# Performance work log

Measured on AMD Instinct MI355X. Metric: run time of the kernel, lower is better.

## Reference

```python
import jax, jax.numpy as jnp
import numpy as np

BRANCH = 8
DEPTH = 4
BATCH = 8192


def _build_tree(b=BRANCH, depth=DEPTH):
    level_sizes = [b ** l for l in range(depth + 1)]
    offsets = np.cumsum([0] + level_sizes)
    E = int(offsets[-1])  # 4681 total nodes (edges)
    parent = np.full(E, -1, dtype=np.int64)
    for l in range(1, depth + 1):
        idx = np.arange(level_sizes[l])
        parent[offsets[l] + idx] = offsets[l - 1] + idx // b
    # Each node's softmax group = its parent's children group; root -> group 0 ('ROOT').
    # Internal nodes occupy indices [0, offsets[depth]), so group id = parent+1.
    seg = np.where(parent < 0, 0, parent + 1).astype(np.int32)
    # path_onehot[i, j] = 1 iff j is an ancestor of i or i itself (path to root)
    P = np.zeros((E, E), dtype=np.float32)
    rows = np.arange(E)
    cur = rows.copy()
    for _ in range(depth + 1):
        P[rows, cur] = 1.0
        cur = np.where(parent[cur] < 0, cur, parent[cur])
    P[rows, cur] = 1.0  # root
    return seg, P


def setup_inputs() -> dict:
    key = jax.random.key(0)
    seg, P = _build_tree()
    E = seg.shape[0]
    inputs = jax.random.normal(key, (BATCH, E), dtype=jnp.float32)
    return {
        "inputs": inputs,
        "segment_ids": jnp.asarray(seg),
        "path_onehot": jnp.asarray(P),
    }


def _cascade_log_softmax(inputs, segment_ids, num_segments):
    # inputs: [B, E]; segmented (per-group) log_softmax along the edge axis.
    xT = inputs.T  # [E, B]
    mx = jax.ops.segment_max(xT, segment_ids, num_segments=num_segments)  # [S, B]
    shifted = xT - mx[segment_ids]
    lse = jnp.log(jax.ops.segment_sum(jnp.exp(shifted), segment_ids,
                                      num_segments=num_segments))  # [S, B]
    return (shifted - lse[segment_ids]).T  # [B, E]


def reference(inputs, segment_ids, path_onehot):
    # final_probabilities: product of conditionals along root-to-node paths
    num_segments = int(jnp.max(segment_ids)) + 1
    log_prob = _cascade_log_softmax(inputs, segment_ids, num_segments)  # [B, E]
    # log p(node) = sum of conditional log-probs over ancestors-or-self
    return jnp.exp(log_prob @ path_onehot.T)  # [B, E]
```

## Files before the change

kernel.cpp:

```cpp
#include <hip/hip_runtime.h>


constexpr int E      = 4681;
constexpr int NGROUP = 585;
constexpr int LDSN   = 1 + NGROUP * 9;

__device__ __forceinline__ int lds_idx(int i) {
    return (i == 0) ? 0 : i + ((i - 1) >> 3);
}

__global__ __launch_bounds__(256) void cascade_kernel(const float* __restrict__ in,
                                                      float* __restrict__ out) {
    __shared__ float a[LDSN];
    const int tid = threadIdx.x;
    const long long rowbase = (long long)blockIdx.x * (long long)E;
    const float* __restrict__ rin  = in  + rowbase;
    float* __restrict__       rout = out + rowbase;

    const int s = (4 - ((int)(rowbase & 3))) & 3;
    if (tid < s) a[lds_idx(tid)] = rin[tid];
    const int nv4 = (E - s) >> 2;
    const float4* __restrict__ rin4 = (const float4*)(rin + s);
    for (int j = tid; j < nv4; j += 256) {
        float4 v = rin4[j];
        int i = s + 4 * j;
        a[lds_idx(i)]     = v.x;
        a[lds_idx(i + 1)] = v.y;
        a[lds_idx(i + 2)] = v.z;
        a[lds_idx(i + 3)] = v.w;
    }
    for (int i = s + 4 * nv4 + tid; i < E; i += 256) a[lds_idx(i)] = rin[i];

    if (tid == 0) a[0] = 0.0f;
    __syncthreads();

    constexpr int OFF[5] = {0, 1, 9, 73, 585};
    #pragma unroll
    for (int l = 0; l < 4; ++l) {
        for (int p = OFF[l] + tid; p < OFF[l + 1]; p += 256) {
            const int cb = 1 + 9 * p;
            float c[8];
            #pragma unroll
            for (int k = 0; k < 8; ++k) c[k] = a[cb + k];
            float m = c[0];
            #pragma unroll
            for (int k = 1; k < 8; ++k) m = fmaxf(m, c[k]);
            float ssum = 0.0f;
            #pragma unroll
            for (int k = 0; k < 8; ++k) ssum += __expf(c[k] - m);
            const float adj = a[lds_idx(p)] - m - __logf(ssum);
            #pragma unroll
            for (int k = 0; k < 8; ++k) a[cb + k] = c[k] + adj;
        }
        __syncthreads();
    }

    if (tid < s) rout[tid] = __expf(a[lds_idx(tid)]);
    float4* __restrict__ rout4 = (float4*)(rout + s);
    for (int j = tid; j < nv4; j += 256) {
        int i = s + 4 * j;
        float4 v;
        v.x = __expf(a[lds_idx(i)]);
        v.y = __expf(a[lds_idx(i + 1)]);
        v.z = __expf(a[lds_idx(i + 2)]);
        v.w = __expf(a[lds_idx(i + 3)]);
        rout4[j] = v;
    }
    for (int i = s + 4 * nv4 + tid; i < E; i += 256) rout[i] = __expf(a[lds_idx(i)]);
}

extern "C" void kernel_launch(void* const* d_in, const int* in_sizes, int n_in,
                              void* d_out, int out_size, void* d_ws, size_t ws_size,
                              hipStream_t stream) {
    const float* in = (const float*)d_in[0];
    float* out = (float*)d_out;
    const int B = in_sizes[0] / E;
    cascade_kernel<<<B, 256, 0, stream>>>(in, out);
}
```

Measured before the change: 303.6 us.

## Parallelize group softmax across lanes with shuffles and async global-to-LDS loads

Replaces the per-thread serial 8-child softmax, which ran level by level, with a lane-parallel pass over all edges at once. Each lane holds one child, and group max and sum come from xor shuffles. The per-group offsets are then propagated down the tree with a small prefix pass over 585 groups. Input rows are loaded directly into LDS with global_load_lds, which drops the padded index mapping. The output is now written as scalar stores instead of float4 stores, which may reduce store efficiency.

```diff
diff --git a/kernel.cpp b/kernel.cpp
--- a/kernel.cpp
+++ b/kernel.cpp
@@ -1,72 +1,66 @@
 #include <hip/hip_runtime.h>
 
 
-constexpr int E      = 4681;
-constexpr int NGROUP = 585;
-constexpr int LDSN   = 1 + NGROUP * 9;
-
-__device__ __forceinline__ int lds_idx(int i) {
-    return (i == 0) ? 0 : i + ((i - 1) >> 3);
-}
+constexpr int E  = 4681;
+constexpr int NG = 585;
 
 __global__ __launch_bounds__(256) void cascade_kernel(const float* __restrict__ in,
                                                       float* __restrict__ out) {
-    __shared__ float a[LDSN];
-    const int tid = threadIdx.x;
+    __shared__ float xs[E];
+    __shared__ float dj[NG];
+    const int tid  = threadIdx.x;
+    const int lane = tid & 63;
     const long long rowbase = (long long)blockIdx.x * (long long)E;
     const float* __restrict__ rin  = in  + rowbase;
     float* __restrict__       rout = out + rowbase;
 
-    const int s = (4 - ((int)(rowbase & 3))) & 3;
-    if (tid < s) a[lds_idx(tid)] = rin[tid];
+    const int s   = (int)((4 - (rowbase & 3)) & 3);
     const int nv4 = (E - s) >> 2;
-    const float4* __restrict__ rin4 = (const float4*)(rin + s);
-    for (int j = tid; j < nv4; j += 256) {
-        float4 v = rin4[j];
-        int i = s + 4 * j;
-        a[lds_idx(i)]     = v.x;
-        a[lds_idx(i + 1)] = v.y;
-        a[lds_idx(i + 2)] = v.z;
-        a[lds_idx(i + 3)] = v.w;
+    const float* vbase = rin + s;
+    const int wbase = tid - lane;
+    #pragma unroll
+    for (int u = 0; u < 5; ++u) {
+        const int f = u * 256 + wbase;
+        if (f < nv4) {
+            const int idx = f + lane;
+            if (idx < nv4) {
+                __builtin_amdgcn_global_load_lds(
+                    (const __attribute__((address_space(1))) void*)(vbase + 4 * idx),
+                    (__attribute__((address_space(3))) void*)(&xs[s + 4 * f]),
+                    16, 0, 0);
+            }
+        }
     }
-    for (int i = s + 4 * nv4 + tid; i < E; i += 256) a[lds_idx(i)] = rin[i];
-
-    if (tid == 0) a[0] = 0.0f;
+    if (tid < s) xs[tid] = rin[tid];
+    const int t0 = s + 4 * nv4;
+    if (tid < E - t0) xs[t0 + tid] = rin[t0 + tid];
     __syncthreads();
 
-    constexpr int OFF[5] = {0, 1, 9, 73, 585};
-    #pragma unroll
-    for (int l = 0; l < 4; ++l) {
-        for (int p = OFF[l] + tid; p < OFF[l + 1]; p += 256) {
-            const int cb = 1 + 9 * p;
-            float c[8];
-            #pragma unroll
-            for (int k = 0; k < 8; ++k) c[k] = a[cb + k];
-            float m = c[0];
-            #pragma unroll
-            for (int k = 1; k < 8; ++k) m = fmaxf(m, c[k]);
-            float ssum = 0.0f;
-            #pragma unroll
-            for (int k = 0; k < 8; ++k) ssum += __expf(c[k] - m);
-            const float adj = a[lds_idx(p)] - m - __logf(ssum);
-            #pragma unroll
-            for (int k = 0; k < 8; ++k) a[cb + k] = c[k] + adj;
-        }
-        __syncthreads();
+    for (int j = tid; j < E - 1; j += 256) {
+        const float v = xs[j + 1];
+        float m = v;
+        m = fmaxf(m, __shfl_xor(m, 1));
+        m = fmaxf(m, __shfl_xor(m, 2));
+        m = fmaxf(m, __shfl_xor(m, 4));
+        float e = __expf(v - m);
+        e += __shfl_xor(e, 1);
+        e += __shfl_xor(e, 2);
+        e += __shfl_xor(e, 4);
+        if ((j & 7) == 0) dj[j >> 3] = -m - __logf(e);
     }
+    __syncthreads();
 
-    if (tid < s) rout[tid] = __expf(a[lds_idx(tid)]);
-    float4* __restrict__ rout4 = (float4*)(rout + s);
-    for (int j = tid; j < nv4; j += 256) {
-        int i = s + 4 * j;
-        float4 v;
-        v.x = __expf(a[lds_idx(i)]);
-        v.y = __expf(a[lds_idx(i + 1)]);
-        v.z = __expf(a[lds_idx(i + 2)]);
-        v.w = __expf(a[lds_idx(i + 3)]);
-        rout4[j] = v;
+    if (tid >= 1 && tid <= 8) dj[tid] += xs[tid] + dj[0];
+    __syncthreads();
+    if (tid >= 9 && tid < 73) dj[tid] += xs[tid] + dj[(tid - 1) >> 3];
+    __syncthreads();
+    for (int p = 73 + tid; p < NG; p += 256) dj[p] += xs[p] + dj[(p - 1) >> 3];
+    __syncthreads();
+
+    for (int j = tid; j < E - 1; j += 256) {
+        rout[j + 1] = __expf(xs[j + 1] + dj[j >> 3]);
     }
-    for (int i = s + 4 * nv4 + tid; i < E; i += 256) rout[i] = __expf(a[lds_idx(i)]);
+    if (tid == 0) rout[0] = 1.0f;
 }
 
 extern "C" void kernel_launch(void* const* d_in, const int* in_sizes, int n_in,
```

Measured after the change: 305.7 us. No clear change (+0.7%).
